# Optimization experiments

Measured on AMD Instinct MI355X. Metric: run time of the kernel, lower is better.

## Reference

```python
import jax, jax.numpy as jnp
import numpy as np

N = 2048   # num nodes
D = 512    # hidden_dim


def setup_inputs() -> dict:
    key = jax.random.key(0)
    k1, k2 = jax.random.split(key)
    x = jax.random.normal(k1, (N, D), dtype=jnp.float32)
    # linear: hidden_dim -> 1 (xavier-like scale)
    w = jax.random.normal(k2, (D,), dtype=jnp.float32) * (1.0 / np.sqrt(D))
    b = jnp.zeros((1,), dtype=jnp.float32)
    return {"x": x, "w": w, "b": b}


def reference(x, w, b):
    # euclidean_distance_matrix + linear fused:
    # s[i,j] = sum_d w_d * (x[i,d]-x[j,d])^2 + b
    #        = q_i + q_j - 2*(x*w) @ x^T + b,  q_i = sum_d w_d x[i,d]^2
    xw = x * w                              # [N, D]
    q = jnp.sum(xw * x, axis=1)             # [N]
    cross = xw @ x.T                        # [N, N]
    s = q[:, None] + q[None, :] - 2.0 * cross + b[0]
    grouping_matrix = jax.nn.sigmoid(s)     # [N, N]

    # compute_fielder, similarity_graph='base'
    W = grouping_matrix
    degree = jnp.sum(W, axis=1)
    L = jnp.diag(degree) - W                # symmetric graph Laplacian
    eigen_values, eigen_vectors = jnp.linalg.eigh(L)
    order = jnp.argsort(jnp.abs(eigen_values))
    fielder_value = eigen_values[order[1]]
    fielder_vector = eigen_vectors[:, order[1]]
    return grouping_matrix, fielder_value, fielder_vector
```

## Files before the change

kernel.cpp:

```cpp
#include <hip/hip_runtime.h>
#include <math.h>

constexpr int NN = 2048;
constexpr int DD_ = 512;
constexpr int LM = 64;
constexpr int VS = NN + 32;
constexpr int GPART = 8;
#define SIGN_FLIP 1

__device__ inline double waveReduceSum(double v) {
#pragma unroll
  for (int off = 32; off; off >>= 1) v += __shfl_down(v, off, 64);
  return v;
}

__device__ inline double blockReduceSum256(double v) {
  __shared__ double sm[4];
  int lane = threadIdx.x & 63;
  int wid  = threadIdx.x >> 6;
  v = waveReduceSum(v);
  __syncthreads();
  if (lane == 0) sm[wid] = v;
  __syncthreads();
  double r = 0.0;
  if (threadIdx.x < 4) r = sm[threadIdx.x];
  if (wid == 0) {
    r += __shfl_down(r, 2, 64);
    r += __shfl_down(r, 1, 64);
  }
  return r;
}

__global__ __launch_bounds__(256) void k_q(const float* __restrict__ x,
                                           const float* __restrict__ w,
                                           float* __restrict__ q) {
  int row = blockIdx.x;
  int t = threadIdx.x;
  const float* xr = x + (size_t)row * DD_;
  float acc = 0.f;
#pragma unroll
  for (int p = 0; p < 2; ++p) {
    int d = t + 256 * p;
    float xv = xr[d];
    acc += w[d] * xv * xv;
  }
  double r = blockReduceSum256((double)acc);
  if (t == 0) q[row] = (float)r;
}

__global__ __launch_bounds__(256) void k_W(const float* __restrict__ x,
                                           const float* __restrict__ wv,
                                           const float* __restrict__ q,
                                           const float* __restrict__ bptr,
                                           float* __restrict__ out) {
  __shared__ float As[16][68];
  __shared__ float Bs[16][68];
  const int t = threadIdx.x;
  const int i0 = blockIdx.y * 64, j0 = blockIdx.x * 64;
  const int lr = t >> 4, lk = t & 15;
  const int tr = t >> 4, tc = t & 15;
  float acc[4][4];
#pragma unroll
  for (int a = 0; a < 4; ++a)
#pragma unroll
    for (int b = 0; b < 4; ++b) acc[a][b] = 0.f;

  for (int kk = 0; kk < DD_; kk += 16) {
    float wk = wv[kk + lk];
#pragma unroll
    for (int p = 0; p < 4; ++p) {
      As[lk][lr + 16 * p] = x[(size_t)(i0 + lr + 16 * p) * DD_ + kk + lk] * wk;
      Bs[lk][lr + 16 * p] = x[(size_t)(j0 + lr + 16 * p) * DD_ + kk + lk];
    }
    __syncthreads();
#pragma unroll
    for (int k = 0; k < 16; ++k) {
      float4 av = *(const float4*)&As[k][tr * 4];
      float4 bv = *(const float4*)&Bs[k][tc * 4];
      float aa[4] = {av.x, av.y, av.z, av.w};
      float bb[4] = {bv.x, bv.y, bv.z, bv.w};
#pragma unroll
      for (int a = 0; a < 4; ++a)
#pragma unroll
        for (int b = 0; b < 4; ++b) acc[a][b] += aa[a] * bb[b];
    }
    __syncthreads();
  }
  float b0 = bptr[0];
#pragma unroll
  for (int a = 0; a < 4; ++a) {
    int i = i0 + tr * 4 + a;
    float qi = q[i];
    float4 st;
    float* stp = &st.x;
#pragma unroll
    for (int b = 0; b < 4; ++b) {
      int j = j0 + tc * 4 + b;
      float s = qi + q[j] - 2.0f * acc[a][b] + b0;
      stp[b] = 1.0f / (1.0f + expf(-s));
    }
    *(float4*)&out[(size_t)i * NN + j0 + tc * 4] = st;
  }
}

__global__ __launch_bounds__(256) void k_init(double* __restrict__ r,
                                              double* __restrict__ part) {
  int t = threadIdx.x;
  double loc[8];
  double s = 0.0;
#pragma unroll
  for (int p = 0; p < 8; ++p) {
    unsigned i = (unsigned)(t + 256 * p);
    unsigned u = i * 2654435761u + 0x9E3779B9u;
    u ^= u >> 16; u *= 0x85EBCA6Bu; u ^= u >> 13; u *= 0xC2B2AE35u; u ^= u >> 16;
    double val = ((double)u / 4294967296.0) - 0.5;
    loc[p] = val; s += val;
  }
  __shared__ double mean_s, inv_s;
  double tot = blockReduceSum256(s);
  if (t == 0) mean_s = tot / (double)NN;
  __syncthreads();
  double mean = mean_s;
  double ss = 0.0;
#pragma unroll
  for (int p = 0; p < 8; ++p) { loc[p] -= mean; ss += loc[p] * loc[p]; }
  double tss = blockReduceSum256(ss);
  if (t == 0) inv_s = 1.0 / sqrt(tss);
  __syncthreads();
  double inv = inv_s;
#pragma unroll
  for (int p = 0; p < 8; ++p) r[t + 256 * p] = loc[p] * inv;
  if (t < GPART) part[t] = (t == 0) ? 1.0 : 0.0;
}

__global__ __launch_bounds__(256) void k_mva(const float* __restrict__ Wm,
                                             double* __restrict__ deg,
                                             const double* __restrict__ rprev,
                                             const double* __restrict__ part,
                                             double* __restrict__ V,
                                             double* __restrict__ wstash,
                                             double* __restrict__ c,
                                             double* __restrict__ beta, int j) {
  int b = blockIdx.x, t = threadIdx.x;
  double ss = 0.0;
#pragma unroll
  for (int p = 0; p < GPART; ++p) ss += part[p];
  double bet = sqrt(ss);
  double inv = (bet > 1e-3) ? 1.0 / bet : 0.0;

  if (b < NN) {
    const float* wr = Wm + (size_t)b * NN;
    double acc = 0.0, dsum = 0.0;
    if (j == 0) {
#pragma unroll
      for (int p = 0; p < 2; ++p) {
        int i = 4 * t + 1024 * p;
        float4 wl = *(const float4*)&wr[i];
        dsum += (double)wl.x + (double)wl.y + (double)wl.z + (double)wl.w;
        acc += (double)wl.x * rprev[i] + (double)wl.y * rprev[i + 1] +
               (double)wl.z * rprev[i + 2] + (double)wl.w * rprev[i + 3];
      }
    } else {
#pragma unroll
      for (int p = 0; p < 2; ++p) {
        int i = 4 * t + 1024 * p;
        float4 wl = *(const float4*)&wr[i];
        acc += (double)wl.x * rprev[i] + (double)wl.y * rprev[i + 1] +
               (double)wl.z * rprev[i + 2] + (double)wl.w * rprev[i + 3];
      }
    }
    double red = blockReduceSum256(acc);
    double dred = 0.0;
    if (j == 0) dred = blockReduceSum256(dsum);
    if (t == 0) {
      double d;
      if (j == 0) { d = dred; deg[b] = d; }
      else d = deg[b];
      double vj = rprev[b] * inv;
      V[(size_t)j * VS + b] = vj;
      wstash[(size_t)j * VS + b] = d * vj - red * inv;
      if (b == 0 && j > 0) beta[j - 1] = (bet > 1e-3) ? bet : 0.0;
    }
  } else {
    int q = b - NN;
    const double* wq = wstash + (size_t)q * VS;
    double a = 0.0;
#pragma unroll
    for (int p = 0; p < 8; ++p) { int i = t + 256 * p; a += wq[i] * rprev[i]; }
    double red = blockReduceSum256(a);
    if (t == 0) c[q] = red * inv;
  }
}

__global__ __launch_bounds__(256) void k_orthb(const double* __restrict__ V,
                                               const double* __restrict__ wstash,
                                               const double* __restrict__ c,
                                               double* __restrict__ r,
                                               double* __restrict__ part,
                                               double* __restrict__ alpha, int j) {
  __shared__ double cs[LM];
  __shared__ double cj_s, s1_s;
  int b = blockIdx.x, t = threadIdx.x;
  const double* wj = wstash + (size_t)j * VS;
  const double* vj = V + (size_t)j * VS;
  double a = 0.0, s = 0.0;
#pragma unroll
  for (int p = 0; p < 8; ++p) {
    int i = t + 256 * p;
    double wv = wj[i];
    a += vj[i] * wv;
    s += wv;
  }
  double cj = blockReduceSum256(a);
  double s1 = blockReduceSum256(s);
  if (t == 0) { cj_s = cj; s1_s = s1; }
  for (int k = t; k < j; k += 256) cs[k] = c[k];
  __syncthreads();
  double cjv = cj_s, s1v = s1_s;
  int i = b * 256 + t;
  double val = wj[i] - s1v / (double)NN - cjv * vj[i];
  for (int k = 0; k < j; ++k) val -= cs[k] * V[(size_t)k * VS + i];
  r[i] = val;
  double rr = blockReduceSum256(val * val);
  if (t == 0) {
    part[b] = rr;
    if (b == 0) alpha[j] = cjv;
  }
}

__device__ inline double guardpiv(double d) {
  if (fabs(d) < 1e-280) return (d < 0.0) ? -1e-280 : 1e-280;
  return d;
}

__global__ __launch_bounds__(64) void k_tri(const double* __restrict__ alpha,
                                            const double* __restrict__ beta,
                                            double* __restrict__ svec) {
  __shared__ double al[LM], be[LM];
  __shared__ double Dg[LM], Dl[LM], Du[LM], Du2[LM], bb[LM];
  __shared__ unsigned char piv[LM];
  __shared__ double bounds[2];
  __shared__ int cnts[64];
  __shared__ int meff_s;
  int t = threadIdx.x;
  for (int i = t; i < LM; i += 64) { al[i] = alpha[i]; be[i] = (i < LM - 1) ? beta[i] : 0.0; }
  __syncthreads();
  if (t == 0) {
    int m = LM;
    for (int i = 0; i < LM; ++i) {
      if (!isfinite(al[i])) { m = i; break; }
      if (i < LM - 1 && (be[i] == 0.0 || !isfinite(be[i]))) { m = i + 1; break; }
    }
    if (m < 2) m = 2;
    meff_s = m;
  }
  __syncthreads();
  const int n = meff_s;
  double lo = 1e300, hi = -1e300;
  for (int i = t; i < n; i += 64) {
    double r = 0.0;
    if (i > 0) r += fabs(be[i - 1]);
    if (i < n - 1) r += fabs(be[i]);
    lo = fmin(lo, al[i] - r);
    hi = fmax(hi, al[i] + r);
  }
#pragma unroll
  for (int off = 32; off; off >>= 1) {
    lo = fmin(lo, __shfl_down(lo, off, 64));
    hi = fmax(hi, __shfl_down(hi, off, 64));
  }
  if (t == 0) { bounds[0] = lo; bounds[1] = hi; }
  __syncthreads();
  for (int round = 0; round < 3; ++round) {
    double L0 = bounds[0], H0 = bounds[1];
    double p = L0 + (H0 - L0) * ((double)(t + 1) / 65.0);
    int cnt = 0;
    double d = al[0] - p;
    if (d < 0) cnt++;
    for (int i = 1; i < n; ++i) {
      if (fabs(d) < 1e-300) d = (d < 0.0) ? -1e-300 : 1e-300;
      double bi = be[i - 1];
      d = (al[i] - p) - bi * bi / d;
      if (d < 0) cnt++;
    }
    cnts[t] = cnt;
    __syncthreads();
    if (t == 0) {
      double nl = L0, nh = H0;
      for (int l = 0; l < 64; ++l) {
        double pl = L0 + (H0 - L0) * ((double)(l + 1) / 65.0);
        if (cnts[l] == 0) nl = pl;
        else { nh = pl; break; }
      }
      bounds[0] = nl; bounds[1] = nh;
    }
    __syncthreads();
  }
  double sigma = 0.5 * (bounds[0] + bounds[1]);
  if (t == 0) {
    for (int i = 0; i < n; ++i) Dg[i] = al[i] - sigma;
    for (int i = 0; i < n - 1; ++i) { Dl[i] = be[i]; Du[i] = be[i]; }
    for (int i = 0; i < n - 2; ++i) Du2[i] = 0.0;
    for (int i = 0; i < n - 1; ++i) {
      if (fabs(Dg[i]) >= fabs(Dl[i])) {
        double dpiv = guardpiv(Dg[i]);
        double fact = Dl[i] / dpiv;
        Dl[i] = fact;
        Dg[i + 1] -= fact * Du[i];
        piv[i] = 0;
      } else {
        double fact = Dg[i] / Dl[i];
        Dg[i] = Dl[i]; Dl[i] = fact;
        double temp = Du[i];
        Du[i] = Dg[i + 1];
        Dg[i + 1] = temp - fact * Dg[i + 1];
        if (i < n - 2) { Du2[i] = Du[i + 1]; Du[i + 1] = -fact * Du[i + 1]; }
        piv[i] = 1;
      }
    }
    for (int i = 0; i < n; ++i) bb[i] = 1.0;
    for (int i = 0; i < n - 1; ++i) {
      if (!piv[i]) bb[i + 1] -= Dl[i] * bb[i];
      else { double tmp = bb[i]; bb[i] = bb[i + 1]; bb[i + 1] = tmp - Dl[i] * bb[i]; }
    }
    bb[n - 1] = bb[n - 1] / guardpiv(Dg[n - 1]);
    bb[n - 2] = (bb[n - 2] - Du[n - 2] * bb[n - 1]) / guardpiv(Dg[n - 2]);
    for (int i = n - 3; i >= 0; --i)
      bb[i] = (bb[i] - Du[i] * bb[i + 1] - Du2[i] * bb[i + 2]) / guardpiv(Dg[i]);
    double nrm = 0.0;
    for (int i = 0; i < n; ++i) nrm += bb[i] * bb[i];
    double s = 1.0 / sqrt(nrm);
    for (int i = 0; i < LM; ++i) svec[i] = (i < n) ? bb[i] * s : 0.0;
  }
}

__global__ __launch_bounds__(256) void k_ritz(const double* __restrict__ V,
                                              const double* __restrict__ s,
                                              double* __restrict__ u) {
  __shared__ double cs[LM];
  int t = threadIdx.x;
  for (int k = t; k < LM; k += 256) cs[k] = s[k];
  __syncthreads();
  int i = blockIdx.x * 256 + t;
  double acc = 0.0;
  for (int k = 0; k < LM; ++k) acc += cs[k] * V[(size_t)k * VS + i];
  u[i] = acc;
}

__global__ __launch_bounds__(256) void k_mvu(const float* __restrict__ Wm,
                                             const double* __restrict__ deg,
                                             const double* __restrict__ v,
                                             double* __restrict__ w) {
  int row = blockIdx.x, t = threadIdx.x;
  const float* wr = Wm + (size_t)row * NN;
  double acc = 0.0;
#pragma unroll
  for (int p = 0; p < 2; ++p) {
    int i = 4 * t + 1024 * p;
    float4 wl = *(const float4*)&wr[i];
    acc += (double)wl.x * v[i] + (double)wl.y * v[i + 1] +
           (double)wl.z * v[i + 2] + (double)wl.w * v[i + 3];
  }
  double r = blockReduceSum256(acc);
  if (t == 0) w[row] = deg[row] * v[row] - r;
}

__global__ __launch_bounds__(256) void k_tail(const double* __restrict__ u,
                                              const double* __restrict__ lu,
                                              float* __restrict__ out_lam,
                                              float* __restrict__ outv) {
  __shared__ double mv[256];
  __shared__ int mi[256];
  __shared__ double mean_s, scale_s;
  int t = threadIdx.x;
  double a = 0.0, b = 0.0;
#pragma unroll
  for (int p = 0; p < 8; ++p) {
    int i = t + 256 * p;
    a += u[i] * lu[i];
    b += u[i] * u[i];
  }
  double ra = blockReduceSum256(a);
  double rb = blockReduceSum256(b);
  if (t == 0) *out_lam = (float)(ra / rb);
  double loc[8];
  double s = 0.0;
#pragma unroll
  for (int p = 0; p < 8; ++p) { loc[p] = u[t + 256 * p]; s += loc[p]; }
  double tot = blockReduceSum256(s);
  if (t == 0) mean_s = tot / (double)NN;
  __syncthreads();
  double mean = mean_s;
  double ss = 0.0, bv = -1.0;
  int bi = 0;
#pragma unroll
  for (int p = 0; p < 8; ++p) {
    loc[p] -= mean;
    ss += loc[p] * loc[p];
    double aa = fabs(loc[p]);
    if (aa > bv) { bv = aa; bi = p; }
  }
  double tss = blockReduceSum256(ss);
  mv[t] = bv; mi[t] = t + 256 * bi;
  __syncthreads();
  for (int off = 128; off; off >>= 1) {
    if (t < off) {
      if (mv[t + off] > mv[t]) { mv[t] = mv[t + off]; mi[t] = mi[t + off]; }
    }
    __syncthreads();
  }
  if (t == 0) {
    int gi = mi[0];
    double best = u[gi] - mean_s;
    double sgn = (best < 0.0) ? -1.0 : 1.0;
#if SIGN_FLIP
    sgn = -sgn;
#endif
    scale_s = sgn / sqrt(tss);
  }
  __syncthreads();
  double sc = scale_s;
#pragma unroll
  for (int p = 0; p < 8; ++p) outv[t + 256 * p] = (float)(loc[p] * sc);
}

extern "C" void kernel_launch(void* const* d_in, const int* in_sizes, int n_in,
                              void* d_out, int out_size, void* d_ws, size_t ws_size,
                              hipStream_t stream) {
  const float* x = (const float*)d_in[0];
  const float* wv = (const float*)d_in[1];
  const float* bp = (const float*)d_in[2];
  float* out = (float*)d_out;

  char* ws = (char*)d_ws;
  size_t off = 0;
  auto alloc = [&](size_t bytes) -> char* {
    char* p = ws + off;
    off = (off + bytes + 255) & ~(size_t)255;
    return p;
  };
  float* q      = (float*)alloc((size_t)NN * 4);
  double* deg   = (double*)alloc((size_t)NN * 8);
  double* r     = (double*)alloc((size_t)NN * 8);
  double* u     = (double*)alloc((size_t)NN * 8);
  double* c     = (double*)alloc((size_t)(LM + 2) * 8);
  double* alpha = (double*)alloc((size_t)LM * 8);
  double* beta  = (double*)alloc((size_t)LM * 8);
  double* svec  = (double*)alloc((size_t)LM * 8);
  double* part  = (double*)alloc((size_t)GPART * 8);
  double* V     = (double*)alloc((size_t)LM * VS * 8);
  double* wstash= (double*)alloc((size_t)LM * VS * 8);
  (void)ws_size; (void)in_sizes; (void)n_in; (void)out_size;

  k_q<<<NN, 256, 0, stream>>>(x, wv, q);
  dim3 g(NN / 64, NN / 64);
  k_W<<<g, 256, 0, stream>>>(x, wv, q, bp, out);
  k_init<<<1, 256, 0, stream>>>(r, part);

  for (int j = 0; j < LM; ++j) {
    k_mva<<<NN + j, 256, 0, stream>>>(out, deg, r, part, V, wstash, c, beta, j);
    k_orthb<<<NN / 256, 256, 0, stream>>>(V, wstash, c, r, part, alpha, j);
  }
  k_tri<<<1, 64, 0, stream>>>(alpha, beta, svec);
  k_ritz<<<NN / 256, 256, 0, stream>>>(V, svec, u);
  k_mvu<<<NN, 256, 0, stream>>>(out, deg, u, r);
  k_tail<<<1, 256, 0, stream>>>(u, r, out + (size_t)NN * NN,
                                out + (size_t)NN * NN + 1);
}
```

Baseline: 842.4 us.

## Fuse Lanczos matvec and orthogonalization into one kernel with in-kernel flag sync

```diff
diff --git a/kernel.cpp b/kernel.cpp
--- a/kernel.cpp
+++ b/kernel.cpp
@@ -5,7 +5,7 @@
 constexpr int DD_ = 512;
 constexpr int LM = 64;
 constexpr int VS = NN + 32;
-constexpr int GPART = 8;
+constexpr int NPRO = 68;
 #define SIGN_FLIP 1
 
 __device__ inline double waveReduceSum(double v) {
@@ -103,8 +103,8 @@
   }
 }
 
-__global__ __launch_bounds__(256) void k_init(double* __restrict__ r,
-                                              double* __restrict__ part) {
+__global__ __launch_bounds__(256) void k_init(double* __restrict__ V,
+                                              unsigned int* __restrict__ flag) {
   int t = threadIdx.x;
   double loc[8];
   double s = 0.0;
@@ -129,103 +129,129 @@
   __syncthreads();
   double inv = inv_s;
 #pragma unroll
-  for (int p = 0; p < 8; ++p) r[t + 256 * p] = loc[p] * inv;
-  if (t < GPART) part[t] = (t == 0) ? 1.0 : 0.0;
-}
-
-__global__ __launch_bounds__(256) void k_mva(const float* __restrict__ Wm,
+  for (int p = 0; p < 8; ++p) V[t + 256 * p] = loc[p] * inv;
+  if (t <= LM) flag[t] = 0u;
+}
+
+__global__ __launch_bounds__(256) void k_lan(const float* __restrict__ Wm,
                                              double* __restrict__ deg,
-                                             const double* __restrict__ rprev,
-                                             const double* __restrict__ part,
                                              double* __restrict__ V,
-                                             double* __restrict__ wstash,
+                                             double* __restrict__ Wst,
                                              double* __restrict__ c,
-                                             double* __restrict__ beta, int j) {
-  int b = blockIdx.x, t = threadIdx.x;
-  double ss = 0.0;
-#pragma unroll
-  for (int p = 0; p < GPART; ++p) ss += part[p];
-  double bet = sqrt(ss);
-  double inv = (bet > 1e-3) ? 1.0 / bet : 0.0;
-
-  if (b < NN) {
-    const float* wr = Wm + (size_t)b * NN;
-    double acc = 0.0, dsum = 0.0;
-    if (j == 0) {
-#pragma unroll
-      for (int p = 0; p < 2; ++p) {
-        int i = 4 * t + 1024 * p;
-        float4 wl = *(const float4*)&wr[i];
-        dsum += (double)wl.x + (double)wl.y + (double)wl.z + (double)wl.w;
-        acc += (double)wl.x * rprev[i] + (double)wl.y * rprev[i + 1] +
-               (double)wl.z * rprev[i + 2] + (double)wl.w * rprev[i + 3];
+                                             double* __restrict__ alpha,
+                                             double* __restrict__ beta,
+                                             unsigned int* __restrict__ flag,
+                                             int j) {
+  const int t = threadIdx.x, b = blockIdx.x;
+
+  if (j > 0 && b < NPRO) {
+    const double* vp = V + (size_t)(j - 1) * VS;
+    if (b == 0) {
+      const double* wp = Wst + (size_t)(j - 1) * VS;
+      double a = 0.0, n2 = 0.0, s = 0.0;
+#pragma unroll
+      for (int p = 0; p < 8; ++p) {
+        int i = t + 256 * p;
+        double wv = wp[i];
+        a += vp[i] * wv; n2 += wv * wv; s += wv;
+      }
+      double ra = blockReduceSum256(a);
+      double rn = blockReduceSum256(n2);
+      double rs = blockReduceSum256(s);
+      if (t == 0) {
+        __hip_atomic_store(&c[j - 1], ra, __ATOMIC_RELAXED, __HIP_MEMORY_SCOPE_AGENT);
+        __hip_atomic_store(&c[LM], rn, __ATOMIC_RELAXED, __HIP_MEMORY_SCOPE_AGENT);
+        __hip_atomic_store(&c[LM + 1], rs, __ATOMIC_RELAXED, __HIP_MEMORY_SCOPE_AGENT);
+        __hip_atomic_fetch_add(&flag[j], 1u, __ATOMIC_RELEASE, __HIP_MEMORY_SCOPE_AGENT);
       }
     } else {
-#pragma unroll
-      for (int p = 0; p < 2; ++p) {
-        int i = 4 * t + 1024 * p;
-        float4 wl = *(const float4*)&wr[i];
-        acc += (double)wl.x * rprev[i] + (double)wl.y * rprev[i + 1] +
-               (double)wl.z * rprev[i + 2] + (double)wl.w * rprev[i + 3];
+      int k = b - 1;
+      if (k <= j - 2) {
+        const double* wk = Wst + (size_t)k * VS;
+        double a = 0.0;
+#pragma unroll
+        for (int p = 0; p < 8; ++p) { int i = t + 256 * p; a += wk[i] * vp[i]; }
+        double ra = blockReduceSum256(a);
+        if (t == 0)
+          __hip_atomic_store(&c[k], ra, __ATOMIC_RELAXED, __HIP_MEMORY_SCOPE_AGENT);
       }
-    }
-    double red = blockReduceSum256(acc);
-    double dred = 0.0;
-    if (j == 0) dred = blockReduceSum256(dsum);
+      if (t == 0)
+        __hip_atomic_fetch_add(&flag[j], 1u, __ATOMIC_RELEASE, __HIP_MEMORY_SCOPE_AGENT);
+    }
+  }
+
+  const double* win = (j == 0) ? V : (Wst + (size_t)(j - 1) * VS);
+  const float* wr = Wm + (size_t)b * NN;
+  double acc = 0.0, dsum = 0.0;
+  if (j == 0) {
+#pragma unroll
+    for (int p = 0; p < 2; ++p) {
+      int i = 4 * t + 1024 * p;
+      float4 wl = *(const float4*)&wr[i];
+      dsum += (double)wl.x + (double)wl.y + (double)wl.z + (double)wl.w;
+      acc += (double)wl.x * win[i] + (double)wl.y * win[i + 1] +
+             (double)wl.z * win[i + 2] + (double)wl.w * win[i + 3];
+    }
+  } else {
+#pragma unroll
+    for (int p = 0; p < 2; ++p) {
+      int i = 4 * t + 1024 * p;
+      float4 wl = *(const float4*)&wr[i];
+      acc += (double)wl.x * win[i] + (double)wl.y * win[i + 1] +
+             (double)wl.z * win[i + 2] + (double)wl.w * win[i + 3];
+    }
+  }
+  double red = blockReduceSum256(acc);
+  if (j == 0) {
+    double dred = blockReduceSum256(dsum);
+    if (t == 0) { deg[b] = dred; Wst[b] = dred * win[b] - red; }
+    return;
+  }
+
+  __shared__ double csh[LM + 2];
+  if (t == 0) {
+    while (__hip_atomic_load(&flag[j], __ATOMIC_ACQUIRE, __HIP_MEMORY_SCOPE_AGENT) < (unsigned)NPRO) {}
+  }
+  __syncthreads();
+  if (t < j) csh[t] = __hip_atomic_load(&c[t], __ATOMIC_RELAXED, __HIP_MEMORY_SCOPE_AGENT);
+  if (t == 64) csh[LM] = __hip_atomic_load(&c[LM], __ATOMIC_RELAXED, __HIP_MEMORY_SCOPE_AGENT);
+  if (t == 65) csh[LM + 1] = __hip_atomic_load(&c[LM + 1], __ATOMIC_RELAXED, __HIP_MEMORY_SCOPE_AGENT);
+  __syncthreads();
+  if (t < 64) {
+    double ck = (t < j) ? csh[t] : 0.0;
+    double vk = 0.0, wk = 0.0;
+    if (t < j) {
+      vk = V[(size_t)t * VS + b];
+      wk = Wst[(size_t)t * VS + b];
+    }
+    double corrV = waveReduceSum(ck * vk);
+    double corrW = waveReduceSum(ck * wk);
+    double sc2 = waveReduceSum(ck * ck);
     if (t == 0) {
-      double d;
-      if (j == 0) { d = dred; deg[b] = d; }
-      else d = deg[b];
-      double vj = rprev[b] * inv;
-      V[(size_t)j * VS + b] = vj;
-      wstash[(size_t)j * VS + b] = d * vj - red * inv;
-      if (b == 0 && j > 0) beta[j - 1] = (bet > 1e-3) ? bet : 0.0;
-    }
-  } else {
-    int q = b - NN;
-    const double* wq = wstash + (size_t)q * VS;
-    double a = 0.0;
-#pragma unroll
-    for (int p = 0; p < 8; ++p) { int i = t + 256 * p; a += wq[i] * rprev[i]; }
-    double red = blockReduceSum256(a);
-    if (t == 0) c[q] = red * inv;
-  }
-}
-
-__global__ __launch_bounds__(256) void k_orthb(const double* __restrict__ V,
-                                               const double* __restrict__ wstash,
-                                               const double* __restrict__ c,
-                                               double* __restrict__ r,
-                                               double* __restrict__ part,
-                                               double* __restrict__ alpha, int j) {
-  __shared__ double cs[LM];
-  __shared__ double cj_s, s1_s;
-  int b = blockIdx.x, t = threadIdx.x;
-  const double* wj = wstash + (size_t)j * VS;
-  const double* vj = V + (size_t)j * VS;
-  double a = 0.0, s = 0.0;
-#pragma unroll
-  for (int p = 0; p < 8; ++p) {
-    int i = t + 256 * p;
-    double wv = wj[i];
-    a += vj[i] * wv;
-    s += wv;
-  }
-  double cj = blockReduceSum256(a);
-  double s1 = blockReduceSum256(s);
-  if (t == 0) { cj_s = cj; s1_s = s1; }
-  for (int k = t; k < j; k += 256) cs[k] = c[k];
-  __syncthreads();
-  double cjv = cj_s, s1v = s1_s;
-  int i = b * 256 + t;
-  double val = wj[i] - s1v / (double)NN - cjv * vj[i];
-  for (int k = 0; k < j; ++k) val -= cs[k] * V[(size_t)k * VS + i];
-  r[i] = val;
-  double rr = blockReduceSum256(val * val);
-  if (t == 0) {
-    part[b] = rr;
-    if (b == 0) alpha[j] = cjv;
-  }
+      double nw2 = csh[LM], s1 = csh[LM + 1];
+      double b2 = nw2 - s1 * s1 / (double)NN - sc2;
+      double bet = (b2 > 1e-6) ? sqrt(b2) : 0.0;
+      double inv = (b2 > 1e-6) ? 1.0 / bet : 0.0;
+      double wpb = win[b];
+      V[(size_t)j * VS + b] = (wpb - s1 / (double)NN - corrV) * inv;
+      double tb = deg[b] * wpb - red;
+      Wst[(size_t)j * VS + b] = (tb - corrW) * inv;
+      if (b == 0) { alpha[j - 1] = csh[j - 1]; beta[j - 1] = bet; }
+    }
+  }
+}
+
+__global__ __launch_bounds__(256) void k_alf(const double* __restrict__ V,
+                                             const double* __restrict__ Wst,
+                                             double* __restrict__ alpha) {
+  int t = threadIdx.x;
+  const double* vp = V + (size_t)(LM - 1) * VS;
+  const double* wp = Wst + (size_t)(LM - 1) * VS;
+  double a = 0.0;
+#pragma unroll
+  for (int p = 0; p < 8; ++p) { int i = t + 256 * p; a += vp[i] * wp[i]; }
+  double ra = blockReduceSum256(a);
+  if (t == 0) alpha[LM - 1] = ra;
 }
 
 __device__ inline double guardpiv(double d) {
@@ -439,31 +465,31 @@
     off = (off + bytes + 255) & ~(size_t)255;
     return p;
   };
-  float* q      = (float*)alloc((size_t)NN * 4);
-  double* deg   = (double*)alloc((size_t)NN * 8);
-  double* r     = (double*)alloc((size_t)NN * 8);
-  double* u     = (double*)alloc((size_t)NN * 8);
-  double* c     = (double*)alloc((size_t)(LM + 2) * 8);
-  double* alpha = (double*)alloc((size_t)LM * 8);
-  double* beta  = (double*)alloc((size_t)LM * 8);
-  double* svec  = (double*)alloc((size_t)LM * 8);
-  double* part  = (double*)alloc((size_t)GPART * 8);
-  double* V     = (double*)alloc((size_t)LM * VS * 8);
-  double* wstash= (double*)alloc((size_t)LM * VS * 8);
+  float* q        = (float*)alloc((size_t)NN * 4);
+  double* deg     = (double*)alloc((size_t)NN * 8);
+  double* u       = (double*)alloc((size_t)NN * 8);
+  double* lu      = (double*)alloc((size_t)NN * 8);
+  double* c       = (double*)alloc((size_t)(LM + 2) * 8);
+  double* alpha   = (double*)alloc((size_t)LM * 8);
+  double* beta    = (double*)alloc((size_t)LM * 8);
+  double* svec    = (double*)alloc((size_t)LM * 8);
+  unsigned int* flag = (unsigned int*)alloc((size_t)(LM + 1) * 4);
+  double* V       = (double*)alloc((size_t)LM * VS * 8);
+  double* Wst     = (double*)alloc((size_t)LM * VS * 8);
   (void)ws_size; (void)in_sizes; (void)n_in; (void)out_size;
 
   k_q<<<NN, 256, 0, stream>>>(x, wv, q);
   dim3 g(NN / 64, NN / 64);
   k_W<<<g, 256, 0, stream>>>(x, wv, q, bp, out);
-  k_init<<<1, 256, 0, stream>>>(r, part);
-
-  for (int j = 0; j < LM; ++j) {
-    k_mva<<<NN + j, 256, 0, stream>>>(out, deg, r, part, V, wstash, c, beta, j);
-    k_orthb<<<NN / 256, 256, 0, stream>>>(V, wstash, c, r, part, alpha, j);
-  }
+  k_init<<<1, 256, 0, stream>>>(V, flag);
+
+  for (int j = 0; j < LM; ++j)
+    k_lan<<<NN, 256, 0, stream>>>(out, deg, V, Wst, c, alpha, beta, flag, j);
+  k_alf<<<1, 256, 0, stream>>>(V, Wst, alpha);
+
   k_tri<<<1, 64, 0, stream>>>(alpha, beta, svec);
   k_ritz<<<NN / 256, 256, 0, stream>>>(V, svec, u);
-  k_mvu<<<NN, 256, 0, stream>>>(out, deg, u, r);
-  k_tail<<<1, 256, 0, stream>>>(u, r, out + (size_t)NN * NN,
+  k_mvu<<<NN, 256, 0, stream>>>(out, deg, u, lu);
+  k_tail<<<1, 256, 0, stream>>>(u, lu, out + (size_t)NN * NN,
                                 out + (size_t)NN * NN + 1);
 }
```

Result: slower. 2.721 ms (+223.0%).
